# Optimization experiments

Measured on AMD Instinct MI355X. Metric: run time of the kernel, lower is better.

## Reference

```python
import jax, jax.numpy as jnp
import numpy as np

H = 16          # N_heads (Attention default)
DH = 32         # d per head (Attention default)
EPS = 1e-5      # torch LayerNorm eps
SCALE = float(1.0 / np.sqrt(DH))


def _ln(z, w, b):
    # LayerNorm over the last TWO dims (normalized_shape=(N_x, channel)), affine w/b of shape [2S, C]
    m = jnp.mean(z, axis=(-2, -1), keepdims=True)
    v = jnp.mean(jnp.square(z - m), axis=(-2, -1), keepdims=True)
    return (z - m) * jax.lax.rsqrt(v + EPS) * w + b


def _attention(a, p):
    # a: [2S, C]. Faithful to source: y = x.clone(), scores are NOT softmaxed (causal_mask=False).
    lx_w, lx_b, ly_w, ly_b, lf_w, lf_b, wq_w, wq_b, wk_w, wk_b, wv_w, wv_b, w1, b1, w2, b2, w3, b3 = p
    L = a.shape[0]
    xn = _ln(a, lx_w, lx_b)
    yn = _ln(a, ly_w, ly_b)
    q = (xn @ wq_w.T + wq_b).reshape(L, H, DH).transpose(1, 0, 2)  # [H, 2S, d]
    k = (yn @ wk_w.T + wk_b).reshape(L, H, DH).transpose(1, 0, 2)
    v = (yn @ wv_w.T + wv_b).reshape(L, H, DH).transpose(1, 0, 2)
    scores = jnp.einsum('hqd,hkd->hqk', q, k) * SCALE               # no softmax in source
    o = jnp.einsum('hqk,hkd->hqd', scores, v).transpose(1, 0, 2).reshape(L, H * DH)
    x1 = a + o @ w1.T + b1
    h = jax.nn.gelu(_ln(x1, lf_w, lf_b) @ w2.T + b2, approximate=False)
    return x1 + h @ w3.T + b3


def _forward(x, params):
    # x: [3, S, S, C]; params are stacked over the idx axis [S, ...] (one Attention per idx, shared across modes)
    S = x.shape[1]
    attn = jax.vmap(_attention, in_axes=(0, 0))
    for m1, m2 in [(0, 1), (2, 0), (1, 2)]:
        a = jnp.concatenate([x[m1], jnp.swapaxes(x[m2], 0, 1)], axis=1)  # [S, 2S, C]
        c = attn(a, params)                                              # [S, 2S, C]
        x = x.at[m1].set(c[:, :S, :])
        x = x.at[m2].set(c[:, S:, :])
    return x


def setup_inputs() -> dict:
    S, C, W = 16, 1024, 4
    D = H * DH   # 512
    L = 2 * S    # 32
    key = jax.random.key(0)
    ks = jax.random.split(key, 8)
    rn = lambda k, shp, s: jax.random.normal(k, shp, dtype=jnp.float32) * s
    return {
        'x': rn(ks[0], (3, S, S, C), 1.0),
        'lx_w': jnp.ones((S, L, C), jnp.float32), 'lx_b': jnp.zeros((S, L, C), jnp.float32),
        'ly_w': jnp.ones((S, L, C), jnp.float32), 'ly_b': jnp.zeros((S, L, C), jnp.float32),
        'lf_w': jnp.ones((S, L, C), jnp.float32), 'lf_b': jnp.zeros((S, L, C), jnp.float32),
        'wq_w': rn(ks[1], (S, D, C), 0.02), 'wq_b': jnp.zeros((S, D), jnp.float32),
        'wk_w': rn(ks[2], (S, D, C), 0.02), 'wk_b': jnp.zeros((S, D), jnp.float32),
        'wv_w': rn(ks[3], (S, D, C), 0.02), 'wv_b': jnp.zeros((S, D), jnp.float32),
        'w1': rn(ks[4], (S, C, D), 0.02), 'b1': jnp.zeros((S, C), jnp.float32),
        'w2': rn(ks[5], (S, W * C, C), 0.02), 'b2': jnp.zeros((S, W * C), jnp.float32),
        'w3': rn(ks[6], (S, C, W * C), 0.02), 'b3': jnp.zeros((S, C), jnp.float32),
    }


def reference(x, lx_w, lx_b, ly_w, ly_b, lf_w, lf_b, wq_w, wq_b, wk_w, wk_b, wv_w, wv_b, w1, b1, w2, b2, w3, b3):
    params = (lx_w, lx_b, ly_w, ly_b, lf_w, lf_b, wq_w, wq_b, wk_w, wk_b, wv_w, wv_b, w1, b1, w2, b2, w3, b3)
    return _forward(x, params)
```

## Files before the change

### kernel.cpp

```cpp
#include <hip/hip_runtime.h>


#define C1024 1024
#define D512  512
#define FF4096 4096
#define NELEM 32768.0f
#define EPSLN 1e-5f
#define QSCALE 0.17677669529663687f
#define LP 258

typedef __attribute__((ext_vector_type(8))) short bf16x8;
typedef __attribute__((ext_vector_type(4))) float f32x4;
typedef unsigned short u16;

__device__ inline u16 f2bf(float f) {
    unsigned u = __float_as_uint(f);
    u += 0x7fffu + ((u >> 16) & 1u);
    return (u16)(u >> 16);
}

__device__ inline bf16x8 cvt8(f32x4 a, f32x4 b) {
    bf16x8 r;
    r[0] = (short)f2bf(a[0]); r[1] = (short)f2bf(a[1]);
    r[2] = (short)f2bf(a[2]); r[3] = (short)f2bf(a[3]);
    r[4] = (short)f2bf(b[0]); r[5] = (short)f2bf(b[1]);
    r[6] = (short)f2bf(b[2]); r[7] = (short)f2bf(b[3]);
    return r;
}

struct Cvt6 {
    const float* s[6];
    u16* d[6];
    int N32[6], kzs[6], base[6];
};
__global__ void __launch_bounds__(256, 4) k_cvt6(Cvt6 a) {
    __shared__ float lds[32 * LP];
    int bid = blockIdx.x;
    int ts = 0;
#pragma unroll
    for (int j = 1; j < 6; ++j) if (bid >= a.base[j]) ts = j;
    int local = bid - a.base[ts];
    int kzs = a.kzs[ts], N32 = a.N32[ts];
    int kz = local % kzs;
    int nt = (local / kzs) % N32;
    int i  = local / (kzs * N32);
    int K = kzs * 256;
    int t = threadIdx.x;
    int row = t >> 3, c8 = t & 7;
    const float* Sp = a.s[ts] + ((size_t)(i * N32 + nt) * 32 + row) * K + kz * 256 + c8 * 4;
    float* Lrow = lds + row * LP + c8 * 4;
#pragma unroll
    for (int j = 0; j < 8; ++j) {
        f32x4 v = *(const f32x4*)(Sp + 32 * j);
        Lrow[32 * j]     = v[0];
        Lrow[32 * j + 1] = v[1];
        Lrow[32 * j + 2] = v[2];
        Lrow[32 * j + 3] = v[3];
    }
    __syncthreads();
    u16* D = a.d[ts] + (((size_t)i * N32 + nt) * (kzs * 8) + kz * 8) * 1024;
#pragma unroll
    for (int p = 0; p < 4; ++p) {
        int o = p * 2048 + t * 8;
        int c  = o >> 10;
        int b  = (o >> 9) & 1;
        int kg = (o >> 7) & 3;
        int lr = (o >> 3) & 15;
        const float* src = lds + (b * 16 + lr) * LP + c * 32 + kg * 8;
        f32x4 lo, hi;
        lo[0] = src[0]; lo[1] = src[1]; lo[2] = src[2]; lo[3] = src[3];
        hi[0] = src[4]; hi[1] = src[5]; hi[2] = src[6]; hi[3] = src[7];
        *(bf16x8*)(D + o) = cvt8(lo, hi);
    }
}

__device__ inline void mmz(const u16* __restrict__ act, const u16* __restrict__ p,
                           int nkk, f32x4& acc0, f32x4& acc1) {
#pragma unroll 4
    for (int j = 0; j < nkk; ++j) {
        bf16x8 aF = *(const bf16x8*)(act + j * 32);
        bf16x8 b0 = *(const bf16x8*)(p + (size_t)j * 1024);
        bf16x8 b1 = *(const bf16x8*)(p + (size_t)j * 1024 + 512);
        acc0 = __builtin_amdgcn_mfma_f32_16x16x32_bf16(aF, b0, acc0, 0, 0, 0);
        acc1 = __builtin_amdgcn_mfma_f32_16x16x32_bf16(aF, b1, acc1, 0, 0, 0);
    }
}

__device__ inline void reduce256(float& s, float& q, int t, float* lds) {
    for (int off = 32; off; off >>= 1) {
        s += __shfl_down(s, off, 64);
        q += __shfl_down(q, off, 64);
    }
    int wv = t >> 6;
    if ((t & 63) == 0) { lds[wv * 2] = s; lds[wv * 2 + 1] = q; }
    __syncthreads();
    if (t == 0) {
        lds[8] = lds[0] + lds[2] + lds[4] + lds[6];
        lds[9] = lds[1] + lds[3] + lds[5] + lds[7];
    }
    __syncthreads();
    s = lds[8]; q = lds[9];
}

__global__ void k_ln1(const float* __restrict__ s1, const float* __restrict__ s2,
                      const float* __restrict__ gw, const float* __restrict__ gb,
                      const float* __restrict__ hw, const float* __restrict__ hb,
                      float* __restrict__ a_buf,
                      u16* __restrict__ xn, u16* __restrict__ yn) {
    __shared__ float lds[10];
    int i = blockIdx.x, cb = blockIdx.y, t = threadIdx.x;
    float s = 0.f, q = 0.f;
#pragma unroll 4
    for (int rr = 0; rr < 32; ++rr) {
        const float* src = (rr < 16)
            ? (s1 + ((i * 16 + rr) << 10))
            : (s2 + (((rr - 16) * 16 + i) << 10));
        f32x4 v = *(const f32x4*)(src + t * 4);
        s += v[0] + v[1] + v[2] + v[3];
        q += v[0]*v[0] + v[1]*v[1] + v[2]*v[2] + v[3]*v[3];
        if ((t >> 5) == cb)
            *(f32x4*)(a_buf + ((i * 32 + rr) << 10) + t * 4) = v;
    }
    reduce256(s, q, t, lds);
    float mean = s * (1.f / NELEM);
    float var = q * (1.f / NELEM) - mean * mean;
    float inv = rsqrtf(var + EPSLN);
    int c = cb * 128 + (t & 31) * 4;
    int r0 = (t >> 5) * 4;
#pragma unroll
    for (int rr = 0; rr < 4; ++rr) {
        int row = r0 + rr;
        const float* src = (row < 16)
            ? (s1 + ((i * 16 + row) << 10))
            : (s2 + (((row - 16) * 16 + i) << 10));
        f32x4 v = *(const f32x4*)(src + c);
        int base = ((i * 32 + row) << 10) + c;
        f32x4 gwv = *(const f32x4*)(gw + base);
        f32x4 gbv = *(const f32x4*)(gb + base);
        f32x4 hwv = *(const f32x4*)(hw + base);
        f32x4 hbv = *(const f32x4*)(hb + base);
        float z0 = (v[0]-mean)*inv, z1 = (v[1]-mean)*inv, z2 = (v[2]-mean)*inv, z3 = (v[3]-mean)*inv;
        uint2 a, b;
        a.x = (unsigned)f2bf(z0*gwv[0]+gbv[0]) | ((unsigned)f2bf(z1*gwv[1]+gbv[1]) << 16);
        a.y = (unsigned)f2bf(z2*gwv[2]+gbv[2]) | ((unsigned)f2bf(z3*gwv[3]+gbv[3]) << 16);
        b.x = (unsigned)f2bf(z0*hwv[0]+hbv[0]) | ((unsigned)f2bf(z1*hwv[1]+hbv[1]) << 16);
        b.y = (unsigned)f2bf(z2*hwv[2]+hbv[2]) | ((unsigned)f2bf(z3*hwv[3]+hbv[3]) << 16);
        *(uint2*)(xn + base) = a;
        *(uint2*)(yn + base) = b;
    }
}

__global__ void k_ln2(const float* __restrict__ x1,
                      const float* __restrict__ gw, const float* __restrict__ gb,
                      u16* __restrict__ out) {
    __shared__ float lds[10];
    int i = blockIdx.x, cb = blockIdx.y, t = threadIdx.x;
    float s = 0.f, q = 0.f;
#pragma unroll 4
    for (int rr = 0; rr < 32; ++rr) {
        f32x4 v = *(const f32x4*)(x1 + ((i * 32 + rr) << 10) + t * 4);
        s += v[0] + v[1] + v[2] + v[3];
        q += v[0]*v[0] + v[1]*v[1] + v[2]*v[2] + v[3]*v[3];
    }
    reduce256(s, q, t, lds);
    float mean = s * (1.f / NELEM);
    float var = q * (1.f / NELEM) - mean * mean;
    float inv = rsqrtf(var + EPSLN);
    int c = cb * 128 + (t & 31) * 4;
    int r0 = (t >> 5) * 4;
#pragma unroll
    for (int rr = 0; rr < 4; ++rr) {
        int base = ((i * 32 + r0 + rr) << 10) + c;
        f32x4 v  = *(const f32x4*)(x1 + base);
        f32x4 gwv = *(const f32x4*)(gw + base);
        f32x4 gbv = *(const f32x4*)(gb + base);
        float z0 = (v[0]-mean)*inv, z1 = (v[1]-mean)*inv, z2 = (v[2]-mean)*inv, z3 = (v[3]-mean)*inv;
        uint2 a;
        a.x = (unsigned)f2bf(z0*gwv[0]+gbv[0]) | ((unsigned)f2bf(z1*gwv[1]+gbv[1]) << 16);
        a.y = (unsigned)f2bf(z2*gwv[2]+gbv[2]) | ((unsigned)f2bf(z3*gwv[3]+gbv[3]) << 16);
        *(uint2*)(out + base) = a;
    }
}

__global__ void __launch_bounds__(512, 4)
k_gemm_qkv(const u16* __restrict__ xn, const u16* __restrict__ yn,
           const u16* __restrict__ wq, const float* __restrict__ wqb,
           const u16* __restrict__ wk, const float* __restrict__ wkb,
           const u16* __restrict__ wv, const float* __restrict__ wvb,
           u16* __restrict__ qo, u16* __restrict__ ko, u16* __restrict__ vT) {
    __shared__ float Pl[2][32][64];
    int bx = blockIdx.x, i = blockIdx.y;
    int w = threadIdx.x >> 6, lane = threadIdx.x & 63;
    int kh = w >> 2, mh = (w >> 1) & 1, wn = w & 1;
    int lr = lane & 15, kg = lane >> 4;
    int sel = bx >> 3;
    int ntl = (bx - sel * 8) * 2 + wn;
    const u16* act = (sel == 0 ? xn : yn) + (i * 32 + mh * 16 + lr) * C1024 + kh * 512 + kg * 8;
    const u16* Wm = (sel == 0 ? wq : (sel == 1 ? wk : wv));
    const u16* p = Wm + (((size_t)i * 16 + ntl) * 32 + kh * 16) * 1024 + lane * 8;
    f32x4 a0 = {0.f, 0.f, 0.f, 0.f}, a1 = {0.f, 0.f, 0.f, 0.f};
    mmz(act, p, 16, a0, a1);
    int m0 = mh * 16 + kg * 4;
#pragma unroll
    for (int r = 0; r < 4; ++r) {
        Pl[kh][m0 + r][wn * 32 + lr] = a0[r];
        Pl[kh][m0 + r][wn * 32 + 16 + lr] = a1[r];
    }
    __syncthreads();
    int t = threadIdx.x;
    int row = t >> 4, c0 = (t & 15) * 4;
    int nloc = bx * 64 - sel * 512 + c0;
    const float* bias = (sel == 0 ? wqb : (sel == 1 ? wkb : wvb)) + i * D512 + nloc;
    float v0 = Pl[0][row][c0]     + Pl[1][row][c0]     + bias[0];
    float v1 = Pl[0][row][c0 + 1] + Pl[1][row][c0 + 1] + bias[1];
    float v2 = Pl[0][row][c0 + 2] + Pl[1][row][c0 + 2] + bias[2];
    float v3 = Pl[0][row][c0 + 3] + Pl[1][row][c0 + 3] + bias[3];
    if (sel == 0) {
        uint2 a;
        a.x = (unsigned)f2bf(v0 * QSCALE) | ((unsigned)f2bf(v1 * QSCALE) << 16);
        a.y = (unsigned)f2bf(v2 * QSCALE) | ((unsigned)f2bf(v3 * QSCALE) << 16);
        *(uint2*)(qo + (i * 32 + row) * D512 + nloc) = a;
    } else if (sel == 1) {
        uint2 a;
        a.x = (unsigned)f2bf(v0) | ((unsigned)f2bf(v1) << 16);
        a.y = (unsigned)f2bf(v2) | ((unsigned)f2bf(v3) << 16);
        *(uint2*)(ko + (i * 32 + row) * D512 + nloc) = a;
    } else {
        int h = nloc >> 5, d = nloc & 31;
        u16* vb = vT + ((i * 16 + h) * 32 + d) * 32 + row;
        vb[0]  = f2bf(v0);
        vb[32] = f2bf(v1);
        vb[64] = f2bf(v2);
        vb[96] = f2bf(v3);
    }
}

__global__ void k_attn(const u16* __restrict__ q, const u16* __restrict__ k,
                       const u16* __restrict__ vT, u16* __restrict__ o) {
    __shared__ __align__(16) u16 Sm[4][32][32];
    int i = blockIdx.x;
    int w = threadIdx.x >> 6, lane = threadIdx.x & 63;
    int h = blockIdx.y * 4 + w;
    int lr = lane & 15, kg = lane >> 4;
    const u16* qb = q + i * 32 * D512 + h * 32 + kg * 8;
    const u16* kb = k + i * 32 * D512 + h * 32 + kg * 8;
    bf16x8 a0 = *(const bf16x8*)(qb + lr * D512);
    bf16x8 a1 = *(const bf16x8*)(qb + (16 + lr) * D512);
    bf16x8 b0 = *(const bf16x8*)(kb + lr * D512);
    bf16x8 b1 = *(const bf16x8*)(kb + (16 + lr) * D512);
    f32x4 z = {0.f, 0.f, 0.f, 0.f};
    f32x4 s00 = __builtin_amdgcn_mfma_f32_16x16x32_bf16(a0, b0, z, 0, 0, 0);
    f32x4 s01 = __builtin_amdgcn_mfma_f32_16x16x32_bf16(a0, b1, z, 0, 0, 0);
    f32x4 s10 = __builtin_amdgcn_mfma_f32_16x16x32_bf16(a1, b0, z, 0, 0, 0);
    f32x4 s11 = __builtin_amdgcn_mfma_f32_16x16x32_bf16(a1, b1, z, 0, 0, 0);
    int mr = kg * 4;
#pragma unroll
    for (int r = 0; r < 4; ++r) {
        Sm[w][mr + r][lr]           = f2bf(s00[r]);
        Sm[w][mr + r][16 + lr]      = f2bf(s01[r]);
        Sm[w][16 + mr + r][lr]      = f2bf(s10[r]);
        Sm[w][16 + mr + r][16 + lr] = f2bf(s11[r]);
    }
    __syncthreads();
    bf16x8 p0 = *(const bf16x8*)&Sm[w][lr][kg * 8];
    bf16x8 p1 = *(const bf16x8*)&Sm[w][16 + lr][kg * 8];
    const u16* vb = vT + (i * 16 + h) * 32 * 32 + kg * 8;
    bf16x8 v0 = *(const bf16x8*)(vb + lr * 32);
    bf16x8 v1 = *(const bf16x8*)(vb + (16 + lr) * 32);
    f32x4 o00 = __builtin_amdgcn_mfma_f32_16x16x32_bf16(p0, v0, z, 0, 0, 0);
    f32x4 o01 = __builtin_amdgcn_mfma_f32_16x16x32_bf16(p0, v1, z, 0, 0, 0);
    f32x4 o10 = __builtin_amdgcn_mfma_f32_16x16x32_bf16(p1, v0, z, 0, 0, 0);
    f32x4 o11 = __builtin_amdgcn_mfma_f32_16x16x32_bf16(p1, v1, z, 0, 0, 0);
#pragma unroll
    for (int r = 0; r < 4; ++r) {
        o[(i * 32 + mr + r) * D512 + h * 32 + lr]           = f2bf(o00[r]);
        o[(i * 32 + mr + r) * D512 + h * 32 + 16 + lr]      = f2bf(o01[r]);
        o[(i * 32 + 16 + mr + r) * D512 + h * 32 + lr]      = f2bf(o10[r]);
        o[(i * 32 + 16 + mr + r) * D512 + h * 32 + 16 + lr] = f2bf(o11[r]);
    }
}

__global__ void __launch_bounds__(512, 4)
k_gemm_w1(const u16* __restrict__ ob, const u16* __restrict__ W,
          const float* __restrict__ bias, const float* __restrict__ a_buf,
          float* __restrict__ x1) {
    __shared__ float Pl[2][32][64];
    int bx = blockIdx.x, i = blockIdx.y;
    int w = threadIdx.x >> 6, lane = threadIdx.x & 63;
    int kh = w >> 2, mh = (w >> 1) & 1, wn = w & 1;
    int lr = lane & 15, kg = lane >> 4;
    int nt = bx * 2 + wn;
    const u16* act = ob + (i * 32 + mh * 16 + lr) * D512 + kh * 256 + kg * 8;
    const u16* p = W + (((size_t)i * 32 + nt) * 16 + kh * 8) * 1024 + lane * 8;
    f32x4 a0 = {0.f, 0.f, 0.f, 0.f}, a1 = {0.f, 0.f, 0.f, 0.f};
    mmz(act, p, 8, a0, a1);
    int m0 = mh * 16 + kg * 4;
#pragma unroll
    for (int r = 0; r < 4; ++r) {
        Pl[kh][m0 + r][wn * 32 + lr] = a0[r];
        Pl[kh][m0 + r][wn * 32 + 16 + lr] = a1[r];
    }
    __syncthreads();
    int t = threadIdx.x;
    int row = t >> 4, c0 = (t & 15) * 4;
    int n = bx * 64 + c0;
    int base = ((i * 32 + row) << 10) + n;
    f32x4 bv = *(const f32x4*)(bias + i * C1024 + n);
    f32x4 av = *(const f32x4*)(a_buf + base);
    f32x4 r;
    r[0] = Pl[0][row][c0]     + Pl[1][row][c0]     + bv[0] + av[0];
    r[1] = Pl[0][row][c0 + 1] + Pl[1][row][c0 + 1] + bv[1] + av[1];
    r[2] = Pl[0][row][c0 + 2] + Pl[1][row][c0 + 2] + bv[2] + av[2];
    r[3] = Pl[0][row][c0 + 3] + Pl[1][row][c0 + 3] + bv[3] + av[3];
    *(f32x4*)(x1 + base) = r;
}

__global__ void __launch_bounds__(256, 4)
k_gemm_w2(const u16* __restrict__ lnf, const u16* __restrict__ W,
          const float* __restrict__ bias, u16* __restrict__ hb) {
    int bx = blockIdx.x, i = blockIdx.y;
    int w = threadIdx.x >> 6, lane = threadIdx.x & 63;
    int mh = w & 1, wn = w >> 1, lr = lane & 15, kg = lane >> 4;
    int nt = bx * 2 + wn;
    const u16* act = lnf + (i * 32 + mh * 16 + lr) * C1024 + kg * 8;
    const u16* p = W + (((size_t)i * 128 + nt) * 32) * 1024 + lane * 8;
    f32x4 a0 = {0.f, 0.f, 0.f, 0.f}, a1 = {0.f, 0.f, 0.f, 0.f};
    mmz(act, p, 32, a0, a1);
    int m0 = mh * 16 + kg * 4;
    int nb = bx * 64 + wn * 32;
    int n0 = nb + lr, n1 = nb + 16 + lr;
    float b0 = bias[i * FF4096 + n0], b1 = bias[i * FF4096 + n1];
#pragma unroll
    for (int r = 0; r < 4; ++r) {
        float t0 = a0[r] + b0;
        float t1 = a1[r] + b1;
        float g0 = 0.5f * t0 * (1.f + erff(t0 * 0.70710678118654752f));
        float g1 = 0.5f * t1 * (1.f + erff(t1 * 0.70710678118654752f));
        hb[(i * 32 + m0 + r) * FF4096 + n0] = f2bf(g0);
        hb[(i * 32 + m0 + r) * FF4096 + n1] = f2bf(g1);
    }
}

__global__ void __launch_bounds__(1024, 4)
k_gemm_w3(const u16* __restrict__ hb, const u16* __restrict__ W,
          const float* __restrict__ bias, const float* __restrict__ x1,
          float* __restrict__ xout, int m1, int m2) {
    __shared__ float Pl[4][32][64];
    int bx = blockIdx.x, i = blockIdx.y;
    int w = threadIdx.x >> 6, lane = threadIdx.x & 63;
    int kq = w >> 2, mh = (w >> 1) & 1, wn = w & 1;
    int lr = lane & 15, kg = lane >> 4;
    int nt = bx * 2 + wn;
    const u16* act = hb + (i * 32 + mh * 16 + lr) * FF4096 + kq * 1024 + kg * 8;
    const u16* p = W + (((size_t)i * 32 + nt) * 128 + kq * 32) * 1024 + lane * 8;
    f32x4 a0 = {0.f, 0.f, 0.f, 0.f}, a1 = {0.f, 0.f, 0.f, 0.f};
    mmz(act, p, 32, a0, a1);
    int m0 = mh * 16 + kg * 4;
#pragma unroll
    for (int r = 0; r < 4; ++r) {
        Pl[kq][m0 + r][wn * 32 + lr] = a0[r];
        Pl[kq][m0 + r][wn * 32 + 16 + lr] = a1[r];
    }
    __syncthreads();
    int t = threadIdx.x;
    int row = t >> 5, c0 = (t & 31) * 2;
    int n = bx * 64 + c0;
    int dst = (row < 16) ? (((m1 * 16 + i) * 16 + row) << 10)
                         : (((m2 * 16 + i) * 16 + (row - 16)) << 10);
    int base = ((i * 32 + row) << 10) + n;
#pragma unroll
    for (int j = 0; j < 2; ++j) {
        float v = Pl[0][row][c0 + j] + Pl[1][row][c0 + j]
                + Pl[2][row][c0 + j] + Pl[3][row][c0 + j]
                + bias[i * C1024 + n + j] + x1[base + j];
        xout[dst + n + j] = v;
    }
}

extern "C" void kernel_launch(void* const* d_in, const int* in_sizes, int n_in,
                              void* d_out, int out_size, void* d_ws, size_t ws_size,
                              hipStream_t stream) {
    const float* x_in = (const float*)d_in[0];
    const float* lx_w = (const float*)d_in[1];
    const float* lx_b = (const float*)d_in[2];
    const float* ly_w = (const float*)d_in[3];
    const float* ly_b = (const float*)d_in[4];
    const float* lf_w = (const float*)d_in[5];
    const float* lf_b = (const float*)d_in[6];
    const float* wq_w = (const float*)d_in[7];
    const float* wq_b = (const float*)d_in[8];
    const float* wk_w = (const float*)d_in[9];
    const float* wk_b = (const float*)d_in[10];
    const float* wv_w = (const float*)d_in[11];
    const float* wv_b = (const float*)d_in[12];
    const float* w1   = (const float*)d_in[13];
    const float* b1   = (const float*)d_in[14];
    const float* w2   = (const float*)d_in[15];
    const float* b2   = (const float*)d_in[16];
    const float* w3   = (const float*)d_in[17];
    const float* b3   = (const float*)d_in[18];

    float* xbuf = (float*)d_out;
    char* ws = (char*)d_ws;
    float* a_buf  = (float*)(ws);
    float* x1_buf = (float*)(ws + (2u << 20));
    u16*   xn     = (u16*)(ws + (4u << 20));
    u16*   yn     = (u16*)(ws + (5u << 20));
    u16*   lnf    = (u16*)(ws + (6u << 20));
    u16*   qb     = (u16*)(ws + (7u << 20));
    u16*   kb     = (u16*)(ws + 7 * (1u << 20) + (1u << 19));
    u16*   vT     = (u16*)(ws + (8u << 20));
    u16*   ob     = (u16*)(ws + 8 * (1u << 20) + (1u << 19));
    u16*   hbuf   = (u16*)(ws + (9u << 20));
    u16*   wq16   = (u16*)(ws + (16u  << 20));
    u16*   wk16   = (u16*)(ws + (32u  << 20));
    u16*   wv16   = (u16*)(ws + (48u  << 20));
    u16*   w1_16  = (u16*)(ws + (64u  << 20));
    u16*   w2_16  = (u16*)(ws + (80u  << 20));
    u16*   w3_16  = (u16*)(ws + (208u << 20));

    Cvt6 ca;
    ca.s[0] = wq_w; ca.d[0] = wq16;  ca.N32[0] = 16;  ca.kzs[0] = 4;  ca.base[0] = 0;
    ca.s[1] = wk_w; ca.d[1] = wk16;  ca.N32[1] = 16;  ca.kzs[1] = 4;  ca.base[1] = 1024;
    ca.s[2] = wv_w; ca.d[2] = wv16;  ca.N32[2] = 16;  ca.kzs[2] = 4;  ca.base[2] = 2048;
    ca.s[3] = w1;   ca.d[3] = w1_16; ca.N32[3] = 32;  ca.kzs[3] = 2;  ca.base[3] = 3072;
    ca.s[4] = w2;   ca.d[4] = w2_16; ca.N32[4] = 128; ca.kzs[4] = 4;  ca.base[4] = 4096;
    ca.s[5] = w3;   ca.d[5] = w3_16; ca.N32[5] = 32;  ca.kzs[5] = 16; ca.base[5] = 12288;
    k_cvt6<<<20480, 256, 0, stream>>>(ca);

    const size_t SLAB = (size_t)16 * 16 * 1024;
    const int modes[3][2] = {{0, 1}, {2, 0}, {1, 2}};
    for (int mi = 0; mi < 3; ++mi) {
        int m1 = modes[mi][0], m2 = modes[mi][1];
        const float* s1 = (mi == 2) ? (xbuf + m1 * SLAB) : (x_in + m1 * SLAB);
        const float* s2 = (mi == 0) ? (x_in + m2 * SLAB) : (xbuf + m2 * SLAB);
        k_ln1<<<dim3(16, 8), 256, 0, stream>>>(s1, s2, lx_w, lx_b, ly_w, ly_b, a_buf, xn, yn);
        k_gemm_qkv<<<dim3(24, 16), 512, 0, stream>>>(xn, yn, wq16, wq_b, wk16, wk_b, wv16, wv_b, qb, kb, vT);
        k_attn<<<dim3(16, 4), 256, 0, stream>>>(qb, kb, vT, ob);
        k_gemm_w1<<<dim3(16, 16), 512, 0, stream>>>(ob, w1_16, b1, a_buf, x1_buf);
        k_ln2<<<dim3(16, 8), 256, 0, stream>>>(x1_buf, lf_w, lf_b, lnf);
        k_gemm_w2<<<dim3(64, 16), 256, 0, stream>>>(lnf, w2_16, b2, hbuf);
        k_gemm_w3<<<dim3(16, 16), 1024, 0, stream>>>(hbuf, w3_16, b3, x1_buf, xbuf, m1, m2);
    }
}
```

Before: 538.3 us.

## Fuse fp32-to-bf16 weight conversion into first-mode GEMMs

Removes the standalone weight conversion kernel. The GEMMs of the first mode now read fp32 weights directly, convert them to bf16 in registers for the MFMA, and write the packed bf16 copy for the later two modes. This saves one full fp32 read and one bf16 read of all weights, plus a launch. In exchange the first-mode GEMMs move twice the weight bytes with strided fp32 row loads, which are less coalesced than the old packed layout.

Result: slower. 578.5 us (+7.5%).

```diff
diff --git a/kernel.cpp b/kernel.cpp
--- a/kernel.cpp
+++ b/kernel.cpp
@@ -7,7 +7,6 @@
 #define NELEM 32768.0f
 #define EPSLN 1e-5f
 #define QSCALE 0.17677669529663687f
-#define LP 258
 
 typedef __attribute__((ext_vector_type(8))) short bf16x8;
 typedef __attribute__((ext_vector_type(4))) float f32x4;
@@ -28,52 +27,6 @@
     return r;
 }
 
-struct Cvt6 {
-    const float* s[6];
-    u16* d[6];
-    int N32[6], kzs[6], base[6];
-};
-__global__ void __launch_bounds__(256, 4) k_cvt6(Cvt6 a) {
-    __shared__ float lds[32 * LP];
-    int bid = blockIdx.x;
-    int ts = 0;
-#pragma unroll
-    for (int j = 1; j < 6; ++j) if (bid >= a.base[j]) ts = j;
-    int local = bid - a.base[ts];
-    int kzs = a.kzs[ts], N32 = a.N32[ts];
-    int kz = local % kzs;
-    int nt = (local / kzs) % N32;
-    int i  = local / (kzs * N32);
-    int K = kzs * 256;
-    int t = threadIdx.x;
-    int row = t >> 3, c8 = t & 7;
-    const float* Sp = a.s[ts] + ((size_t)(i * N32 + nt) * 32 + row) * K + kz * 256 + c8 * 4;
-    float* Lrow = lds + row * LP + c8 * 4;
-#pragma unroll
-    for (int j = 0; j < 8; ++j) {
-        f32x4 v = *(const f32x4*)(Sp + 32 * j);
-        Lrow[32 * j]     = v[0];
-        Lrow[32 * j + 1] = v[1];
-        Lrow[32 * j + 2] = v[2];
-        Lrow[32 * j + 3] = v[3];
-    }
-    __syncthreads();
-    u16* D = a.d[ts] + (((size_t)i * N32 + nt) * (kzs * 8) + kz * 8) * 1024;
-#pragma unroll
-    for (int p = 0; p < 4; ++p) {
-        int o = p * 2048 + t * 8;
-        int c  = o >> 10;
-        int b  = (o >> 9) & 1;
-        int kg = (o >> 7) & 3;
-        int lr = (o >> 3) & 15;
-        const float* src = lds + (b * 16 + lr) * LP + c * 32 + kg * 8;
-        f32x4 lo, hi;
-        lo[0] = src[0]; lo[1] = src[1]; lo[2] = src[2]; lo[3] = src[3];
-        hi[0] = src[4]; hi[1] = src[5]; hi[2] = src[6]; hi[3] = src[7];
-        *(bf16x8*)(D + o) = cvt8(lo, hi);
-    }
-}
-
 __device__ inline void mmz(const u16* __restrict__ act, const u16* __restrict__ p,
                            int nkk, f32x4& acc0, f32x4& acc1) {
 #pragma unroll 4
@@ -81,6 +34,29 @@
         bf16x8 aF = *(const bf16x8*)(act + j * 32);
         bf16x8 b0 = *(const bf16x8*)(p + (size_t)j * 1024);
         bf16x8 b1 = *(const bf16x8*)(p + (size_t)j * 1024 + 512);
+        acc0 = __builtin_amdgcn_mfma_f32_16x16x32_bf16(aF, b0, acc0, 0, 0, 0);
+        acc1 = __builtin_amdgcn_mfma_f32_16x16x32_bf16(aF, b1, acc1, 0, 0, 0);
+    }
+}
+
+__device__ inline void mmz_cvt(const u16* __restrict__ act,
+                               const float* __restrict__ w32, int K,
+                               u16* __restrict__ w16c, bool st,
+                               int nkk, f32x4& acc0, f32x4& acc1) {
+    const float* w32b = w32 + (size_t)16 * K;
+#pragma unroll 2
+    for (int j = 0; j < nkk; ++j) {
+        bf16x8 aF = *(const bf16x8*)(act + j * 32);
+        f32x4 l0 = *(const f32x4*)(w32 + j * 32);
+        f32x4 h0 = *(const f32x4*)(w32 + j * 32 + 4);
+        f32x4 l1 = *(const f32x4*)(w32b + j * 32);
+        f32x4 h1 = *(const f32x4*)(w32b + j * 32 + 4);
+        bf16x8 b0 = cvt8(l0, h0);
+        bf16x8 b1 = cvt8(l1, h1);
+        if (st) {
+            *(bf16x8*)(w16c + (size_t)j * 1024) = b0;
+            *(bf16x8*)(w16c + (size_t)j * 1024 + 512) = b1;
+        }
         acc0 = __builtin_amdgcn_mfma_f32_16x16x32_bf16(aF, b0, acc0, 0, 0, 0);
         acc1 = __builtin_amdgcn_mfma_f32_16x16x32_bf16(aF, b1, acc1, 0, 0, 0);
     }
@@ -182,11 +158,14 @@
     }
 }
 
+template<bool M0>
 __global__ void __launch_bounds__(512, 4)
 k_gemm_qkv(const u16* __restrict__ xn, const u16* __restrict__ yn,
-           const u16* __restrict__ wq, const float* __restrict__ wqb,
-           const u16* __restrict__ wk, const float* __restrict__ wkb,
-           const u16* __restrict__ wv, const float* __restrict__ wvb,
+           u16* __restrict__ wq, const float* __restrict__ wqb,
+           u16* __restrict__ wk, const float* __restrict__ wkb,
+           u16* __restrict__ wv, const float* __restrict__ wvb,
+           const float* __restrict__ wq32, const float* __restrict__ wk32,
+           const float* __restrict__ wv32,
            u16* __restrict__ qo, u16* __restrict__ ko, u16* __restrict__ vT) {
     __shared__ float Pl[2][32][64];
     int bx = blockIdx.x, i = blockIdx.y;
@@ -196,10 +175,16 @@
     int sel = bx >> 3;
     int ntl = (bx - sel * 8) * 2 + wn;
     const u16* act = (sel == 0 ? xn : yn) + (i * 32 + mh * 16 + lr) * C1024 + kh * 512 + kg * 8;
-    const u16* Wm = (sel == 0 ? wq : (sel == 1 ? wk : wv));
-    const u16* p = Wm + (((size_t)i * 16 + ntl) * 32 + kh * 16) * 1024 + lane * 8;
+    u16* Wm = (sel == 0 ? wq : (sel == 1 ? wk : wv));
+    u16* p = Wm + (((size_t)i * 16 + ntl) * 32 + kh * 16) * 1024 + lane * 8;
     f32x4 a0 = {0.f, 0.f, 0.f, 0.f}, a1 = {0.f, 0.f, 0.f, 0.f};
-    mmz(act, p, 16, a0, a1);
+    if constexpr (M0) {
+        const float* W32 = (sel == 0 ? wq32 : (sel == 1 ? wk32 : wv32));
+        const float* pw = W32 + ((size_t)i * 512 + ntl * 32 + lr) * 1024 + kh * 512 + kg * 8;
+        mmz_cvt(act, pw, 1024, p, mh == 0, 16, a0, a1);
+    } else {
+        mmz(act, p, 16, a0, a1);
+    }
     int m0 = mh * 16 + kg * 4;
 #pragma unroll
     for (int r = 0; r < 4; ++r) {
@@ -280,10 +265,11 @@
     }
 }
 
+template<bool M0>
 __global__ void __launch_bounds__(512, 4)
-k_gemm_w1(const u16* __restrict__ ob, const u16* __restrict__ W,
-          const float* __restrict__ bias, const float* __restrict__ a_buf,
-          float* __restrict__ x1) {
+k_gemm_w1(const u16* __restrict__ ob, u16* __restrict__ W,
+          const float* __restrict__ W32, const float* __restrict__ bias,
+          const float* __restrict__ a_buf, float* __restrict__ x1) {
     __shared__ float Pl[2][32][64];
     int bx = blockIdx.x, i = blockIdx.y;
     int w = threadIdx.x >> 6, lane = threadIdx.x & 63;
@@ -291,9 +277,14 @@
     int lr = lane & 15, kg = lane >> 4;
     int nt = bx * 2 + wn;
     const u16* act = ob + (i * 32 + mh * 16 + lr) * D512 + kh * 256 + kg * 8;
-    const u16* p = W + (((size_t)i * 32 + nt) * 16 + kh * 8) * 1024 + lane * 8;
+    u16* p = W + (((size_t)i * 32 + nt) * 16 + kh * 8) * 1024 + lane * 8;
     f32x4 a0 = {0.f, 0.f, 0.f, 0.f}, a1 = {0.f, 0.f, 0.f, 0.f};
-    mmz(act, p, 8, a0, a1);
+    if constexpr (M0) {
+        const float* pw = W32 + ((size_t)i * 1024 + nt * 32 + lr) * 512 + kh * 256 + kg * 8;
+        mmz_cvt(act, pw, 512, p, mh == 0, 8, a0, a1);
+    } else {
+        mmz(act, p, 8, a0, a1);
+    }
     int m0 = mh * 16 + kg * 4;
 #pragma unroll
     for (int r = 0; r < 4; ++r) {
@@ -315,17 +306,24 @@
     *(f32x4*)(x1 + base) = r;
 }
 
+template<bool M0>
 __global__ void __launch_bounds__(256, 4)
-k_gemm_w2(const u16* __restrict__ lnf, const u16* __restrict__ W,
-          const float* __restrict__ bias, u16* __restrict__ hb) {
+k_gemm_w2(const u16* __restrict__ lnf, u16* __restrict__ W,
+          const float* __restrict__ W32, const float* __restrict__ bias,
+          u16* __restrict__ hb) {
     int bx = blockIdx.x, i = blockIdx.y;
     int w = threadIdx.x >> 6, lane = threadIdx.x & 63;
     int mh = w & 1, wn = w >> 1, lr = lane & 15, kg = lane >> 4;
     int nt = bx * 2 + wn;
     const u16* act = lnf + (i * 32 + mh * 16 + lr) * C1024 + kg * 8;
-    const u16* p = W + (((size_t)i * 128 + nt) * 32) * 1024 + lane * 8;
+    u16* p = W + (((size_t)i * 128 + nt) * 32) * 1024 + lane * 8;
     f32x4 a0 = {0.f, 0.f, 0.f, 0.f}, a1 = {0.f, 0.f, 0.f, 0.f};
-    mmz(act, p, 32, a0, a1);
+    if constexpr (M0) {
+        const float* pw = W32 + ((size_t)i * 4096 + nt * 32 + lr) * 1024 + kg * 8;
+        mmz_cvt(act, pw, 1024, p, mh == 0, 32, a0, a1);
+    } else {
+        mmz(act, p, 32, a0, a1);
+    }
     int m0 = mh * 16 + kg * 4;
     int nb = bx * 64 + wn * 32;
     int n0 = nb + lr, n1 = nb + 16 + lr;
@@ -341,10 +339,11 @@
     }
 }
 
+template<bool M0>
 __global__ void __launch_bounds__(1024, 4)
-k_gemm_w3(const u16* __restrict__ hb, const u16* __restrict__ W,
-          const float* __restrict__ bias, const float* __restrict__ x1,
-          float* __restrict__ xout, int m1, int m2) {
+k_gemm_w3(const u16* __restrict__ hb, u16* __restrict__ W,
+          const float* __restrict__ W32, const float* __restrict__ bias,
+          const float* __restrict__ x1, float* __restrict__ xout, int m1, int m2) {
     __shared__ float Pl[4][32][64];
     int bx = blockIdx.x, i = blockIdx.y;
     int w = threadIdx.x >> 6, lane = threadIdx.x & 63;
@@ -352,9 +351,14 @@
     int lr = lane & 15, kg = lane >> 4;
     int nt = bx * 2 + wn;
     const u16* act = hb + (i * 32 + mh * 16 + lr) * FF4096 + kq * 1024 + kg * 8;
-    const u16* p = W + (((size_t)i * 32 + nt) * 128 + kq * 32) * 1024 + lane * 8;
+    u16* p = W + (((size_t)i * 32 + nt) * 128 + kq * 32) * 1024 + lane * 8;
     f32x4 a0 = {0.f, 0.f, 0.f, 0.f}, a1 = {0.f, 0.f, 0.f, 0.f};
-    mmz(act, p, 32, a0, a1);
+    if constexpr (M0) {
+        const float* pw = W32 + ((size_t)i * 1024 + nt * 32 + lr) * 4096 + kq * 1024 + kg * 8;
+        mmz_cvt(act, pw, 4096, p, mh == 0, 32, a0, a1);
+    } else {
+        mmz(act, p, 32, a0, a1);
+    }
     int m0 = mh * 16 + kg * 4;
 #pragma unroll
     for (int r = 0; r < 4; ++r) {
@@ -419,15 +423,6 @@
     u16*   w2_16  = (u16*)(ws + (80u  << 20));
     u16*   w3_16  = (u16*)(ws + (208u << 20));
 
-    Cvt6 ca;
-    ca.s[0] = wq_w; ca.d[0] = wq16;  ca.N32[0] = 16;  ca.kzs[0] = 4;  ca.base[0] = 0;
-    ca.s[1] = wk_w; ca.d[1] = wk16;  ca.N32[1] = 16;  ca.kzs[1] = 4;  ca.base[1] = 1024;
-    ca.s[2] = wv_w; ca.d[2] = wv16;  ca.N32[2] = 16;  ca.kzs[2] = 4;  ca.base[2] = 2048;
-    ca.s[3] = w1;   ca.d[3] = w1_16; ca.N32[3] = 32;  ca.kzs[3] = 2;  ca.base[3] = 3072;
-    ca.s[4] = w2;   ca.d[4] = w2_16; ca.N32[4] = 128; ca.kzs[4] = 4;  ca.base[4] = 4096;
-    ca.s[5] = w3;   ca.d[5] = w3_16; ca.N32[5] = 32;  ca.kzs[5] = 16; ca.base[5] = 12288;
-    k_cvt6<<<20480, 256, 0, stream>>>(ca);
-
     const size_t SLAB = (size_t)16 * 16 * 1024;
     const int modes[3][2] = {{0, 1}, {2, 0}, {1, 2}};
     for (int mi = 0; mi < 3; ++mi) {
@@ -435,11 +430,31 @@
         const float* s1 = (mi == 2) ? (xbuf + m1 * SLAB) : (x_in + m1 * SLAB);
         const float* s2 = (mi == 0) ? (x_in + m2 * SLAB) : (xbuf + m2 * SLAB);
         k_ln1<<<dim3(16, 8), 256, 0, stream>>>(s1, s2, lx_w, lx_b, ly_w, ly_b, a_buf, xn, yn);
-        k_gemm_qkv<<<dim3(24, 16), 512, 0, stream>>>(xn, yn, wq16, wq_b, wk16, wk_b, wv16, wv_b, qb, kb, vT);
+        if (mi == 0) {
+            k_gemm_qkv<true><<<dim3(24, 16), 512, 0, stream>>>(
+                xn, yn, wq16, wq_b, wk16, wk_b, wv16, wv_b,
+                wq_w, wk_w, wv_w, qb, kb, vT);
+        } else {
+            k_gemm_qkv<false><<<dim3(24, 16), 512, 0, stream>>>(
+                xn, yn, wq16, wq_b, wk16, wk_b, wv16, wv_b,
+                nullptr, nullptr, nullptr, qb, kb, vT);
+        }
         k_attn<<<dim3(16, 4), 256, 0, stream>>>(qb, kb, vT, ob);
-        k_gemm_w1<<<dim3(16, 16), 512, 0, stream>>>(ob, w1_16, b1, a_buf, x1_buf);
+        if (mi == 0) {
+            k_gemm_w1<true><<<dim3(16, 16), 512, 0, stream>>>(ob, w1_16, w1, b1, a_buf, x1_buf);
+        } else {
+            k_gemm_w1<false><<<dim3(16, 16), 512, 0, stream>>>(ob, w1_16, nullptr, b1, a_buf, x1_buf);
+        }
         k_ln2<<<dim3(16, 8), 256, 0, stream>>>(x1_buf, lf_w, lf_b, lnf);
-        k_gemm_w2<<<dim3(64, 16), 256, 0, stream>>>(lnf, w2_16, b2, hbuf);
-        k_gemm_w3<<<dim3(16, 16), 1024, 0, stream>>>(hbuf, w3_16, b3, x1_buf, xbuf, m1, m2);
-    }
-}
+        if (mi == 0) {
+            k_gemm_w2<true><<<dim3(64, 16), 256, 0, stream>>>(lnf, w2_16, w2, b2, hbuf);
+        } else {
+            k_gemm_w2<false><<<dim3(64, 16), 256, 0, stream>>>(lnf, w2_16, nullptr, b2, hbuf);
+        }
+        if (mi == 0) {
+            k_gemm_w3<true><<<dim3(16, 16), 1024, 0, stream>>>(hbuf, w3_16, w3, b3, x1_buf, xbuf, m1, m2);
+        } else {
+            k_gemm_w3<false><<<dim3(16, 16), 1024, 0, stream>>>(hbuf, w3_16, nullptr, b3, x1_buf, xbuf, m1, m2);
+        }
+    }
+}
```

## Interleave weight conversion chunks with first-mode GEMMs for cache reuse

Applied to the files above, without the earlier changes.

The single fused fp32-to-bf16 conversion kernel for all six weight tensors is split into separate launches. In the first mode each launch runs right before the kernel that uses its output. W2 and W3 are each converted in two halves, and each half is followed by a GEMM over just those output columns. The intent is for the freshly written bf16 weights to still sit in the last-level cache when the GEMM reads them, avoiding a trip to HBM. The cost is more kernel launches plus smaller grids for the first-mode W2/W3 GEMMs. Everything stays on one stream, so no compute overlaps.

Result: slower. 562.4 us (+4.5%).

```diff
diff --git a/kernel.cpp b/kernel.cpp
--- a/kernel.cpp
+++ b/kernel.cpp
@@ -28,26 +28,18 @@
     return r;
 }
 
-struct Cvt6 {
-    const float* s[6];
-    u16* d[6];
-    int N32[6], kzs[6], base[6];
-};
-__global__ void __launch_bounds__(256, 4) k_cvt6(Cvt6 a) {
+__global__ void __launch_bounds__(256, 4)
+k_cvt(const float* __restrict__ S, u16* __restrict__ D,
+      int N32, int kzs, int ntOff, int ntCnt) {
     __shared__ float lds[32 * LP];
     int bid = blockIdx.x;
-    int ts = 0;
-#pragma unroll
-    for (int j = 1; j < 6; ++j) if (bid >= a.base[j]) ts = j;
-    int local = bid - a.base[ts];
-    int kzs = a.kzs[ts], N32 = a.N32[ts];
-    int kz = local % kzs;
-    int nt = (local / kzs) % N32;
-    int i  = local / (kzs * N32);
+    int kz = bid % kzs;
+    int nt = ntOff + (bid / kzs) % ntCnt;
+    int i  = bid / (kzs * ntCnt);
     int K = kzs * 256;
     int t = threadIdx.x;
     int row = t >> 3, c8 = t & 7;
-    const float* Sp = a.s[ts] + ((size_t)(i * N32 + nt) * 32 + row) * K + kz * 256 + c8 * 4;
+    const float* Sp = S + ((size_t)(i * N32 + nt) * 32 + row) * K + kz * 256 + c8 * 4;
     float* Lrow = lds + row * LP + c8 * 4;
 #pragma unroll
     for (int j = 0; j < 8; ++j) {
@@ -58,7 +50,7 @@
         Lrow[32 * j + 3] = v[3];
     }
     __syncthreads();
-    u16* D = a.d[ts] + (((size_t)i * N32 + nt) * (kzs * 8) + kz * 8) * 1024;
+    u16* Dp = D + (((size_t)i * N32 + nt) * (kzs * 8) + kz * 8) * 1024;
 #pragma unroll
     for (int p = 0; p < 4; ++p) {
         int o = p * 2048 + t * 8;
@@ -70,7 +62,7 @@
         f32x4 lo, hi;
         lo[0] = src[0]; lo[1] = src[1]; lo[2] = src[2]; lo[3] = src[3];
         hi[0] = src[4]; hi[1] = src[5]; hi[2] = src[6]; hi[3] = src[7];
-        *(bf16x8*)(D + o) = cvt8(lo, hi);
+        *(bf16x8*)(Dp + o) = cvt8(lo, hi);
     }
 }
 
@@ -317,8 +309,8 @@
 
 __global__ void __launch_bounds__(256, 4)
 k_gemm_w2(const u16* __restrict__ lnf, const u16* __restrict__ W,
-          const float* __restrict__ bias, u16* __restrict__ hb) {
-    int bx = blockIdx.x, i = blockIdx.y;
+          const float* __restrict__ bias, u16* __restrict__ hb, int bxoff) {
+    int bx = blockIdx.x + bxoff, i = blockIdx.y;
     int w = threadIdx.x >> 6, lane = threadIdx.x & 63;
     int mh = w & 1, wn = w >> 1, lr = lane & 15, kg = lane >> 4;
     int nt = bx * 2 + wn;
@@ -344,9 +336,9 @@
 __global__ void __launch_bounds__(1024, 4)
 k_gemm_w3(const u16* __restrict__ hb, const u16* __restrict__ W,
           const float* __restrict__ bias, const float* __restrict__ x1,
-          float* __restrict__ xout, int m1, int m2) {
+          float* __restrict__ xout, int m1, int m2, int bxoff) {
     __shared__ float Pl[4][32][64];
-    int bx = blockIdx.x, i = blockIdx.y;
+    int bx = blockIdx.x + bxoff, i = blockIdx.y;
     int w = threadIdx.x >> 6, lane = threadIdx.x & 63;
     int kq = w >> 2, mh = (w >> 1) & 1, wn = w & 1;
     int lr = lane & 15, kg = lane >> 4;
@@ -419,27 +411,35 @@
     u16*   w2_16  = (u16*)(ws + (80u  << 20));
     u16*   w3_16  = (u16*)(ws + (208u << 20));
 
-    Cvt6 ca;
-    ca.s[0] = wq_w; ca.d[0] = wq16;  ca.N32[0] = 16;  ca.kzs[0] = 4;  ca.base[0] = 0;
-    ca.s[1] = wk_w; ca.d[1] = wk16;  ca.N32[1] = 16;  ca.kzs[1] = 4;  ca.base[1] = 1024;
-    ca.s[2] = wv_w; ca.d[2] = wv16;  ca.N32[2] = 16;  ca.kzs[2] = 4;  ca.base[2] = 2048;
-    ca.s[3] = w1;   ca.d[3] = w1_16; ca.N32[3] = 32;  ca.kzs[3] = 2;  ca.base[3] = 3072;
-    ca.s[4] = w2;   ca.d[4] = w2_16; ca.N32[4] = 128; ca.kzs[4] = 4;  ca.base[4] = 4096;
-    ca.s[5] = w3;   ca.d[5] = w3_16; ca.N32[5] = 32;  ca.kzs[5] = 16; ca.base[5] = 12288;
-    k_cvt6<<<20480, 256, 0, stream>>>(ca);
-
     const size_t SLAB = (size_t)16 * 16 * 1024;
     const int modes[3][2] = {{0, 1}, {2, 0}, {1, 2}};
     for (int mi = 0; mi < 3; ++mi) {
         int m1 = modes[mi][0], m2 = modes[mi][1];
         const float* s1 = (mi == 2) ? (xbuf + m1 * SLAB) : (x_in + m1 * SLAB);
         const float* s2 = (mi == 0) ? (x_in + m2 * SLAB) : (xbuf + m2 * SLAB);
+        if (mi == 0) {
+            k_cvt<<<1024, 256, 0, stream>>>(wq_w, wq16, 16, 4, 0, 16);
+            k_cvt<<<1024, 256, 0, stream>>>(wk_w, wk16, 16, 4, 0, 16);
+            k_cvt<<<1024, 256, 0, stream>>>(wv_w, wv16, 16, 4, 0, 16);
+            k_cvt<<<1024, 256, 0, stream>>>(w1,   w1_16, 32, 2, 0, 32);
+        }
         k_ln1<<<dim3(16, 8), 256, 0, stream>>>(s1, s2, lx_w, lx_b, ly_w, ly_b, a_buf, xn, yn);
         k_gemm_qkv<<<dim3(24, 16), 512, 0, stream>>>(xn, yn, wq16, wq_b, wk16, wk_b, wv16, wv_b, qb, kb, vT);
         k_attn<<<dim3(16, 4), 256, 0, stream>>>(qb, kb, vT, ob);
         k_gemm_w1<<<dim3(16, 16), 512, 0, stream>>>(ob, w1_16, b1, a_buf, x1_buf);
         k_ln2<<<dim3(16, 8), 256, 0, stream>>>(x1_buf, lf_w, lf_b, lnf);
-        k_gemm_w2<<<dim3(64, 16), 256, 0, stream>>>(lnf, w2_16, b2, hbuf);
-        k_gemm_w3<<<dim3(16, 16), 1024, 0, stream>>>(hbuf, w3_16, b3, x1_buf, xbuf, m1, m2);
-    }
-}
+        if (mi == 0) {
+            k_cvt<<<4096, 256, 0, stream>>>(w2, w2_16, 128, 4, 0, 64);
+            k_gemm_w2<<<dim3(32, 16), 256, 0, stream>>>(lnf, w2_16, b2, hbuf, 0);
+            k_cvt<<<4096, 256, 0, stream>>>(w2, w2_16, 128, 4, 64, 64);
+            k_gemm_w2<<<dim3(32, 16), 256, 0, stream>>>(lnf, w2_16, b2, hbuf, 32);
+            k_cvt<<<4096, 256, 0, stream>>>(w3, w3_16, 32, 16, 0, 16);
+            k_gemm_w3<<<dim3(8, 16), 1024, 0, stream>>>(hbuf, w3_16, b3, x1_buf, xbuf, m1, m2, 0);
+            k_cvt<<<4096, 256, 0, stream>>>(w3, w3_16, 32, 16, 16, 16);
+            k_gemm_w3<<<dim3(8, 16), 1024, 0, stream>>>(hbuf, w3_16, b3, x1_buf, xbuf, m1, m2, 8);
+        } else {
+            k_gemm_w2<<<dim3(64, 16), 256, 0, stream>>>(lnf, w2_16, b2, hbuf, 0);
+            k_gemm_w3<<<dim3(16, 16), 1024, 0, stream>>>(hbuf, w3_16, b3, x1_buf, xbuf, m1, m2, 0);
+        }
+    }
+}
```
